# Kernel tuning notes

Hardware: AMD Instinct MI355X
Metric: run time of the kernel (lower is better)

## Reference

```python
import jax, jax.numpy as jnp
import numpy as np

NUM_HEADS = 16
HEAD_DIM = 64  # hidden_size 1024 / 16 heads


def setup_inputs() -> dict:
    key = jax.random.key(0)
    ks = jax.random.split(key, 9)
    B, T, H = 8, 4096, 1024
    s = 1.0 / np.sqrt(H)
    return {
        "hidden_states": jax.random.normal(ks[0], (B, T + 1, H), jnp.float32),
        "cell_state": jax.random.normal(ks[1], (B, H), jnp.float32),
        "Wq": jax.random.normal(ks[2], (H, H), jnp.float32) * s,
        "bq": jax.random.normal(ks[3], (H,), jnp.float32) * 0.02,
        "Wk": jax.random.normal(ks[4], (H, H), jnp.float32) * s,
        "bk": jax.random.normal(ks[5], (H,), jnp.float32) * 0.02,
        "Wv": jax.random.normal(ks[6], (H, H), jnp.float32) * s,
        "bv": jax.random.normal(ks[7], (H,), jnp.float32) * 0.02,
        "attention_mask": jax.random.randint(ks[8], (B, T), 0, 2, jnp.int32),
        "t": T,
    }


def reference(hidden_states, cell_state, Wq, bq, Wk, bk, Wv, bv, attention_mask, t):
    B, _, H = hidden_states.shape
    nh, hd = NUM_HEADS, HEAD_DIM
    # single-query projection: [B, H] -> [B, nh, hd]
    q = (cell_state @ Wq.T + bq).reshape(B, nh, hd)
    # key/value over first t positions: [B, t, H] -> [B, t, nh, hd]
    kv_in = hidden_states[:, :-1]
    k = (kv_in @ Wk.T + bk).reshape(B, t, nh, hd)
    v = (kv_in @ Wv.T + bv).reshape(B, t, nh, hd)
    # GEMV-like scores: [B, nh, t]
    scores = jnp.einsum("bhd,bthd->bht", q, k) / np.sqrt(hd)
    # mask out positions where attention_mask == 0 (intended semantics of
    # inf * eq(mask, 0) in the original, expressed without -inf*0 NaNs)
    mask_add = jnp.where(attention_mask == 0, -jnp.inf, 0.0)[:, None, :]
    probs = jax.nn.softmax(scores + mask_add, axis=-1)
    # dropout is identity in eval mode
    ctx = jnp.einsum("bht,bthd->bhd", probs, v)  # [B, nh, hd]
    return ctx.reshape(B, nh * hd)  # squeeze of [B, 1, H]
```

## Files before the change

kernel.cpp:

```cpp
#include <hip/hip_runtime.h>
#include <math.h>

#define BB 8
#define TT 4096
#define TP1 4097
#define HH 1024
#define NHD 16

__device__ __forceinline__ float dot4(const float4& a, const float4& b) {
  return a.x*b.x + a.y*b.y + a.z*b.z + a.w*b.w;
}

__global__ __launch_bounds__(256) void k_q(const float* __restrict__ cell,
                                           const float* __restrict__ Wq,
                                           const float* __restrict__ bq,
                                           float* __restrict__ qbuf) {
  __shared__ float cs[BB * HH];
  int tid = threadIdx.x;
  #pragma unroll
  for (int m = 0; m < 8; m++) {
    int idx4 = tid + (m << 8);
    ((float4*)cs)[idx4] = ((const float4*)cell)[idx4];
  }
  __syncthreads();
  int jj = tid >> 6, lane = tid & 63;
  int j = blockIdx.x * 4 + jj;
  float acc[BB];
  #pragma unroll
  for (int b = 0; b < BB; b++) acc[b] = 0.f;
  #pragma unroll
  for (int k = 0; k < 4; k++) {
    int i = (k << 8) + (lane << 2);
    float4 w = *(const float4*)&Wq[(size_t)j * HH + i];
    #pragma unroll
    for (int b = 0; b < BB; b++) acc[b] += dot4(w, *(const float4*)&cs[b * HH + i]);
  }
  #pragma unroll
  for (int b = 0; b < BB; b++) {
    acc[b] += __shfl_xor(acc[b], 1);  acc[b] += __shfl_xor(acc[b], 2);
    acc[b] += __shfl_xor(acc[b], 4);  acc[b] += __shfl_xor(acc[b], 8);
    acc[b] += __shfl_xor(acc[b], 16); acc[b] += __shfl_xor(acc[b], 32);
  }
  if (lane == 0) {
    float bqv = bq[j];
    #pragma unroll
    for (int b = 0; b < BB; b++) qbuf[b * HH + j] = 0.125f * (acc[b] + bqv);
  }
}

__global__ __launch_bounds__(256) void k_qwk(const float* __restrict__ qbuf,
                                             const float* __restrict__ Wk,
                                             const float* __restrict__ bk,
                                             float* __restrict__ qWkT,
                                             float* __restrict__ qbk) {
  __shared__ float q_s[BB * 64];
  __shared__ float red[4 * 64 * 9];
  int tid = threadIdx.x;
  int h = blockIdx.x >> 4, ic = blockIdx.x & 15;
  if (tid < 128) {
    int b = tid >> 4, dq = tid & 15;
    ((float4*)q_s)[tid] = ((const float4*)qbuf)[(b << 8) + (h << 4) + dq];
  }
  __syncthreads();
  int dg = tid >> 6, lane = tid & 63;
  int i = (ic << 6) + lane;
  float acc[BB];
  #pragma unroll
  for (int b = 0; b < BB; b++) acc[b] = 0.f;
  #pragma unroll
  for (int dd = 0; dd < 16; dd++) {
    int d = (dg << 4) + dd;
    float wk = Wk[(size_t)((h << 6) + d) * HH + i];
    #pragma unroll
    for (int b = 0; b < BB; b++) acc[b] += q_s[(b << 6) + d] * wk;
  }
  #pragma unroll
  for (int b = 0; b < BB; b++) red[((dg << 6) + lane) * 9 + b] = acc[b];
  __syncthreads();
  #pragma unroll
  for (int r = 0; r < 2; r++) {
    int o = tid + (r << 8);
    int il = o >> 3, b = o & 7;
    float s = 0.f;
    #pragma unroll
    for (int g = 0; g < 4; g++) s += red[((g << 6) + il) * 9 + b];
    qWkT[((size_t)(b << 10) + (ic << 6) + il) * NHD + h] = s;
  }
  if (ic == 0 && tid < 8) {
    float s = 0.f;
    for (int d = 0; d < 64; d++) s += q_s[(tid << 6) + d] * bk[(h << 6) + d];
    qbk[tid * NHD + h] = s;
  }
}

#define QT_OFF   0
#define KV_OFF   16384
#define E_OFF    32768
#define RED_OFF  33024
#define RED2_OFF 34048
#define QBK_OFF  34112
#define MSK_OFF  34128

__global__ __launch_bounds__(256, 1) void k_sctx(const float* __restrict__ hid,
                                                 const float* __restrict__ qWkT,
                                                 const float* __restrict__ qbk,
                                                 const int* __restrict__ mask,
                                                 float* __restrict__ ctxp,
                                                 float* __restrict__ Spart) {
  __shared__ float S[34192];
  int tid = threadIdx.x;
  int b = blockIdx.x >> 6, g = blockIdx.x & 63;
  int t0 = g << 6;
  int kq = tid >> 4, rg4 = tid & 15;
  int kqm = kq & 3;

  #pragma unroll
  for (int m = 0; m < 16; m++) {
    int idx = tid + (m << 8);
    float4 v = ((const float4*)qWkT)[((size_t)b << 12) + idx];
    *(float4*)&S[QT_OFF + (idx << 2)] = v;
  }
  if (tid < NHD) S[QBK_OFF + tid] = qbk[b * NHD + tid];
  if (tid < 64) S[MSK_OFF + tid] = (float)mask[b * TT + t0 + tid];

  const float* src = hid + ((size_t)b * TP1 + t0) * HH;
  float4 stg[16];
  #pragma unroll
  for (int m = 0; m < 16; m++)
    stg[m] = *(const float4*)&src[(size_t)m * HH + (tid << 2)];

  float4 acc4[16];
  #pragma unroll
  for (int h = 0; h < 16; h++) acc4[h] = make_float4(0.f, 0.f, 0.f, 0.f);
  float sp = 0.f;

  #pragma unroll 1
  for (int tt = 0; tt < 4; tt++) {
    #pragma unroll
    for (int m = 0; m < 16; m++)
      *(float4*)&S[KV_OFF + (((m << 8) + (tid ^ m)) << 2)] = stg[m];
    __syncthreads();

    float accs[16];
    #pragma unroll
    for (int k = 0; k < 16; k++) accs[k] = 0.f;
    #pragma unroll
    for (int qq = 0; qq < 16; qq++) {
      int q = (kq << 4) + qq;
      float4 kvq = *(const float4*)&S[KV_OFF + (((rg4 << 8) + (q ^ rg4)) << 2)];
      #pragma unroll
      for (int c = 0; c < 4; c++) {
        float kvv = (&kvq.x)[c];
        int i16 = ((q << 2) + c) << 4;
        #pragma unroll
        for (int j = 0; j < 4; j++) {
          int s = j ^ kqm;
          float4 qv = *(const float4*)&S[QT_OFF + i16 + (s << 2)];
          accs[(j << 2) + 0] += kvv * qv.x;
          accs[(j << 2) + 1] += kvv * qv.y;
          accs[(j << 2) + 2] += kvv * qv.z;
          accs[(j << 2) + 3] += kvv * qv.w;
        }
      }
    }
    {
      float tmp[16];
      #pragma unroll
      for (int j = 0; j < 4; j++)
        #pragma unroll
        for (int c = 0; c < 4; c++)
          tmp[(j << 2) + c] = __shfl_xor(accs[((j ^ 1) << 2) + c], 16);
      #pragma unroll
      for (int k = 0; k < 16; k++) accs[k] += tmp[k];
      #pragma unroll
      for (int j = 0; j < 4; j++)
        #pragma unroll
        for (int c = 0; c < 4; c++)
          tmp[(j << 2) + c] = __shfl_xor(accs[((j ^ 2) << 2) + c], 32);
      #pragma unroll
      for (int k = 0; k < 16; k++) accs[k] += tmp[k];
    }
    if ((tid & 48) == 0) {
      int w = tid >> 6;
      #pragma unroll
      for (int j = 0; j < 4; j++)
        *(float4*)&S[RED_OFF + (w << 8) + (rg4 << 4) + (j << 2)] =
            make_float4(accs[(j << 2)], accs[(j << 2) + 1],
                        accs[(j << 2) + 2], accs[(j << 2) + 3]);
    }
    __syncthreads();

    {
      int rge = tid >> 4, he = tid & 15;
      float sv = S[RED_OFF + (rge << 4) + he] + S[RED_OFF + 256 + (rge << 4) + he] +
                 S[RED_OFF + 512 + (rge << 4) + he] + S[RED_OFF + 768 + (rge << 4) + he];
      sv += S[QBK_OFF + he];
      float mkf = S[MSK_OFF + (tt << 4) + rge];
      float ev = (mkf != 0.f) ? __expf(sv) : 0.f;
      S[E_OFF + (rge << 4) + he] = ev;
      sp += ev;
    }
    __syncthreads();

    if (tt < 3) {
      const float* s2 = src + ((size_t)((tt + 1) << 4)) * HH;
      #pragma unroll
      for (int m = 0; m < 16; m++)
        stg[m] = *(const float4*)&s2[(size_t)m * HH + (tid << 2)];
    }

    #pragma unroll
    for (int r = 0; r < 16; r++) {
      float4 kvq = *(const float4*)&S[KV_OFF + (((r << 8) + (tid ^ r)) << 2)];
      float4 e0 = *(const float4*)&S[E_OFF + (r << 4)];
      float4 e1 = *(const float4*)&S[E_OFF + (r << 4) + 4];
      float4 e2 = *(const float4*)&S[E_OFF + (r << 4) + 8];
      float4 e3 = *(const float4*)&S[E_OFF + (r << 4) + 12];
      #define PVH(hh, ev) \
        acc4[hh].x += kvq.x * (ev); acc4[hh].y += kvq.y * (ev); \
        acc4[hh].z += kvq.z * (ev); acc4[hh].w += kvq.w * (ev);
      PVH(0, e0.x)  PVH(1, e0.y)  PVH(2, e0.z)  PVH(3, e0.w)
      PVH(4, e1.x)  PVH(5, e1.y)  PVH(6, e1.z)  PVH(7, e1.w)
      PVH(8, e2.x)  PVH(9, e2.y)  PVH(10, e2.z) PVH(11, e2.w)
      PVH(12, e3.x) PVH(13, e3.y) PVH(14, e3.z) PVH(15, e3.w)
      #undef PVH
    }
    __syncthreads();
  }

  {
    float* cp = ctxp + ((((size_t)b * 64 + g) * 16) << 10) + (tid << 2);
    #pragma unroll
    for (int h = 0; h < 16; h++)
      *(float4*)&cp[(size_t)h << 10] = acc4[h];
  }

  {
    sp += __shfl_xor(sp, 16);
    sp += __shfl_xor(sp, 32);
    int w = tid >> 6;
    if ((tid & 48) == 0) S[RED2_OFF + (w << 4) + (tid & 15)] = sp;
  }
  __syncthreads();
  if (tid < 16) {
    float s = S[RED2_OFF + tid] + S[RED2_OFF + 16 + tid] +
              S[RED2_OFF + 32 + tid] + S[RED2_OFF + 48 + tid];
    Spart[(((size_t)b << 6) + g) * NHD + tid] = s;
  }
}

__global__ void k_sinv(const float* __restrict__ Spart, float* __restrict__ Sinv) {
  int tid = threadIdx.x;
  int b = tid >> 4, h = tid & 15;
  float s = 0.f;
  #pragma unroll 8
  for (int c = 0; c < 64; c++) s += Spart[(size_t)((b << 6) + c) * NHD + h];
  Sinv[tid] = 1.f / s;
}

__global__ __launch_bounds__(256) void k_reduce(const float* __restrict__ ctxp,
                                                float* __restrict__ ctxin) {
  int tid = threadIdx.x;
  int b = blockIdx.x >> 4, h = blockIdx.x & 15;
  const float4* cp4 = (const float4*)ctxp;
  float4 s = make_float4(0.f, 0.f, 0.f, 0.f);
  #pragma unroll 8
  for (int g = 0; g < 64; g++) {
    float4 v = cp4[((((size_t)b * 64 + g) * 16 + h) << 8) + tid];
    s.x += v.x; s.y += v.y; s.z += v.z; s.w += v.w;
  }
  ((float4*)ctxin)[(((size_t)(b << 4) + h) << 8) + tid] = s;
}

__global__ __launch_bounds__(256) void k_out(const float* __restrict__ Wv,
                                             const float* __restrict__ bv,
                                             const float* __restrict__ ctxin,
                                             const float* __restrict__ Sinv,
                                             float* __restrict__ out) {
  __shared__ float cs[BB * HH];
  int tid = threadIdx.x;
  int h = blockIdx.x >> 4;
  int j0 = blockIdx.x * 4;
  #pragma unroll
  for (int m = 0; m < 8; m++) {
    int idx4 = tid + (m << 8);
    int b = idx4 >> 8, i4 = idx4 & 255;
    ((float4*)cs)[idx4] = ((const float4*)ctxin)[(((b << 4) + h) << 8) + i4];
  }
  __syncthreads();
  int jj = tid >> 6, lane = tid & 63;
  int j = j0 + jj;
  float acc[BB];
  #pragma unroll
  for (int b = 0; b < BB; b++) acc[b] = 0.f;
  #pragma unroll
  for (int k = 0; k < 4; k++) {
    int i = (k << 8) + (lane << 2);
    float4 w = *(const float4*)&Wv[(size_t)j * HH + i];
    #pragma unroll
    for (int b = 0; b < BB; b++) acc[b] += dot4(w, *(const float4*)&cs[b * HH + i]);
  }
  #pragma unroll
  for (int b = 0; b < BB; b++) {
    acc[b] += __shfl_xor(acc[b], 1);  acc[b] += __shfl_xor(acc[b], 2);
    acc[b] += __shfl_xor(acc[b], 4);  acc[b] += __shfl_xor(acc[b], 8);
    acc[b] += __shfl_xor(acc[b], 16); acc[b] += __shfl_xor(acc[b], 32);
  }
  if (lane == 0) {
    float bvj = bv[j];
    #pragma unroll
    for (int b = 0; b < BB; b++)
      out[b * HH + j] = Sinv[b * NHD + h] * acc[b] + bvj;
  }
}

extern "C" void kernel_launch(void* const* d_in, const int* in_sizes, int n_in,
                              void* d_out, int out_size, void* d_ws, size_t ws_size,
                              hipStream_t stream) {
  const float* hid  = (const float*)d_in[0];
  const float* cell = (const float*)d_in[1];
  const float* Wq   = (const float*)d_in[2];
  const float* bq   = (const float*)d_in[3];
  const float* Wk   = (const float*)d_in[4];
  const float* bk   = (const float*)d_in[5];
  const float* Wv   = (const float*)d_in[6];
  const float* bv   = (const float*)d_in[7];
  const int*  mask  = (const int*)d_in[8];
  float* out = (float*)d_out;

  float* ws = (float*)d_ws;
  float* qbuf    = ws;
  float* qWkT    = ws + 8192;
  float* qbk     = ws + 139264;
  float* Spart   = ws + 139392;
  float* Sinv    = ws + 147584;
  float* ctxin   = ws + 147712;
  float* ctxp    = ws + 278784;

  hipLaunchKernelGGL(k_q,      dim3(256), dim3(256), 0, stream, cell, Wq, bq, qbuf);
  hipLaunchKernelGGL(k_qwk,    dim3(256), dim3(256), 0, stream, qbuf, Wk, bk, qWkT, qbk);
  hipLaunchKernelGGL(k_sctx,   dim3(512), dim3(256), 0, stream, hid, qWkT, qbk, mask, ctxp, Spart);
  hipLaunchKernelGGL(k_sinv,   dim3(1),   dim3(128), 0, stream, Spart, Sinv);
  hipLaunchKernelGGL(k_reduce, dim3(128), dim3(256), 0, stream, ctxp, ctxin);
  hipLaunchKernelGGL(k_out,    dim3(256), dim3(256), 0, stream, Wv, bv, ctxin, Sinv, out);
}
```

Before: 307.5 us.

## Restructure score/context kernel into two passes with 512-thread blocks

Rewrites k_sctx so each block first computes scores over all 64 positions, streaming 256-column chunks of hidden states, with 8 waves each taking a slice of the reduction dimension. qWkT is now read directly from global memory instead of being staged in LDS. Scores are then reduced across waves, exponentiated and masked, and a second pass re-streams the hidden-state chunks to accumulate context using only 4 of the 8 waves. This frees LDS and raises occupancy, at the cost of reading hidden states twice (probably served from cache) and leaving half the waves idle in the context pass.

```diff
diff --git a/kernel.cpp b/kernel.cpp
--- a/kernel.cpp
+++ b/kernel.cpp
@@ -93,159 +93,151 @@
   }
 }
 
-#define QT_OFF   0
-#define KV_OFF   16384
-#define E_OFF    32768
-#define RED_OFF  33024
-#define RED2_OFF 34048
-#define QBK_OFF  34112
-#define MSK_OFF  34128
-
-__global__ __launch_bounds__(256, 1) void k_sctx(const float* __restrict__ hid,
+__global__ __launch_bounds__(512, 4) void k_sctx(const float* __restrict__ hid,
                                                  const float* __restrict__ qWkT,
                                                  const float* __restrict__ qbk,
                                                  const int* __restrict__ mask,
                                                  float* __restrict__ ctxp,
                                                  float* __restrict__ Spart) {
-  __shared__ float S[34192];
+  __shared__ float KV[16640];
+  __shared__ float E[1280];
   int tid = threadIdx.x;
   int b = blockIdx.x >> 6, g = blockIdx.x & 63;
   int t0 = g << 6;
-  int kq = tid >> 4, rg4 = tid & 15;
-  int kqm = kq & 3;
-
-  #pragma unroll
-  for (int m = 0; m < 16; m++) {
-    int idx = tid + (m << 8);
-    float4 v = ((const float4*)qWkT)[((size_t)b << 12) + idx];
-    *(float4*)&S[QT_OFF + (idx << 2)] = v;
-  }
-  if (tid < NHD) S[QBK_OFF + tid] = qbk[b * NHD + tid];
-  if (tid < 64) S[MSK_OFF + tid] = (float)mask[b * TT + t0 + tid];
-
+  int w = __builtin_amdgcn_readfirstlane(tid >> 6);
+  int lane = tid & 63;
   const float* src = hid + ((size_t)b * TP1 + t0) * HH;
-  float4 stg[16];
-  #pragma unroll
-  for (int m = 0; m < 16; m++)
-    stg[m] = *(const float4*)&src[(size_t)m * HH + (tid << 2)];
-
-  float4 acc4[16];
-  #pragma unroll
-  for (int h = 0; h < 16; h++) acc4[h] = make_float4(0.f, 0.f, 0.f, 0.f);
-  float sp = 0.f;
-
-  #pragma unroll 1
-  for (int tt = 0; tt < 4; tt++) {
-    #pragma unroll
-    for (int m = 0; m < 16; m++)
-      *(float4*)&S[KV_OFF + (((m << 8) + (tid ^ m)) << 2)] = stg[m];
+
+  int sr = tid >> 3, si8 = tid & 7;
+  const float* gs = src + (size_t)sr * HH + (si8 << 2);
+  float* kvw = KV + sr * 260 + (si8 << 2);
+
+  float4 stg[8];
+  #pragma unroll
+  for (int m = 0; m < 8; m++) stg[m] = *(const float4*)(gs + (m << 5));
+  #pragma unroll
+  for (int m = 0; m < 8; m++) *(float4*)(kvw + (m << 5)) = stg[m];
+  __syncthreads();
+
+  float acc[16];
+  #pragma unroll
+  for (int h = 0; h < 16; h++) acc[h] = 0.f;
+  const float* qb = qWkT + ((size_t)b << 14);
+  const float* kvr = KV + lane * 260 + (w << 5);
+
+  for (int c = 0; c < 4; c++) {
+    if (c < 3) {
+      const float* gs2 = gs + ((c + 1) << 8);
+      #pragma unroll
+      for (int m = 0; m < 8; m++) stg[m] = *(const float4*)(gs2 + (m << 5));
+    }
+    int i0 = (c << 8) + (w << 5);
+    #pragma unroll
+    for (int s = 0; s < 8; s++) {
+      float4 kvq = *(const float4*)(kvr + (s << 2));
+      const float* qp = qb + ((size_t)(i0 + (s << 2)) << 4);
+      #pragma unroll
+      for (int ii = 0; ii < 4; ii++) {
+        float kvv = (ii == 0) ? kvq.x : (ii == 1) ? kvq.y : (ii == 2) ? kvq.z : kvq.w;
+        const float* qi = qp + (ii << 4);
+        float4 q0 = *(const float4*)(qi);
+        float4 q1 = *(const float4*)(qi + 4);
+        float4 q2 = *(const float4*)(qi + 8);
+        float4 q3 = *(const float4*)(qi + 12);
+        acc[0]  += kvv * q0.x;  acc[1]  += kvv * q0.y;
+        acc[2]  += kvv * q0.z;  acc[3]  += kvv * q0.w;
+        acc[4]  += kvv * q1.x;  acc[5]  += kvv * q1.y;
+        acc[6]  += kvv * q1.z;  acc[7]  += kvv * q1.w;
+        acc[8]  += kvv * q2.x;  acc[9]  += kvv * q2.y;
+        acc[10] += kvv * q2.z;  acc[11] += kvv * q2.w;
+        acc[12] += kvv * q3.x;  acc[13] += kvv * q3.y;
+        acc[14] += kvv * q3.z;  acc[15] += kvv * q3.w;
+      }
+    }
     __syncthreads();
-
-    float accs[16];
-    #pragma unroll
-    for (int k = 0; k < 16; k++) accs[k] = 0.f;
-    #pragma unroll
-    for (int qq = 0; qq < 16; qq++) {
-      int q = (kq << 4) + qq;
-      float4 kvq = *(const float4*)&S[KV_OFF + (((rg4 << 8) + (q ^ rg4)) << 2)];
-      #pragma unroll
-      for (int c = 0; c < 4; c++) {
-        float kvv = (&kvq.x)[c];
-        int i16 = ((q << 2) + c) << 4;
-        #pragma unroll
-        for (int j = 0; j < 4; j++) {
-          int s = j ^ kqm;
-          float4 qv = *(const float4*)&S[QT_OFF + i16 + (s << 2)];
-          accs[(j << 2) + 0] += kvv * qv.x;
-          accs[(j << 2) + 1] += kvv * qv.y;
-          accs[(j << 2) + 2] += kvv * qv.z;
-          accs[(j << 2) + 3] += kvv * qv.w;
-        }
+    if (c < 3) {
+      #pragma unroll
+      for (int m = 0; m < 8; m++) *(float4*)(kvw + (m << 5)) = stg[m];
+    }
+    __syncthreads();
+  }
+
+  #pragma unroll
+  for (int m = 0; m < 8; m++) stg[m] = *(const float4*)(gs + (m << 5));
+
+  {
+    float* rp = KV + w * 1088 + lane * 17;
+    #pragma unroll
+    for (int h = 0; h < 16; h++) rp[h] = acc[h];
+  }
+  __syncthreads();
+
+  {
+    float s1 = 0.f, s2 = 0.f;
+    #pragma unroll
+    for (int ww = 0; ww < 8; ww++) {
+      s1 += KV[ww * 1088 + lane * 17 + w];
+      s2 += KV[ww * 1088 + lane * 17 + w + 8];
+    }
+    s1 += qbk[b * NHD + w];
+    s2 += qbk[b * NHD + w + 8];
+    int mk = mask[b * TT + t0 + lane];
+    float e1 = mk ? __expf(s1) : 0.f;
+    float e2 = mk ? __expf(s2) : 0.f;
+    E[lane * 20 + w] = e1;
+    E[lane * 20 + w + 8] = e2;
+    float sp1 = e1, sp2 = e2;
+    #pragma unroll
+    for (int m2 = 1; m2 < 64; m2 <<= 1) {
+      sp1 += __shfl_xor(sp1, m2);
+      sp2 += __shfl_xor(sp2, m2);
+    }
+    if (lane == 0) {
+      Spart[(((size_t)b << 6) + g) * NHD + w] = sp1;
+      Spart[(((size_t)b << 6) + g) * NHD + w + 8] = sp2;
+    }
+  }
+  __syncthreads();
+
+  #pragma unroll
+  for (int m = 0; m < 8; m++) *(float4*)(kvw + (m << 5)) = stg[m];
+  __syncthreads();
+
+  int hq = w & 3;
+  for (int c = 0; c < 4; c++) {
+    if (c < 3) {
+      const float* gs2 = gs + ((c + 1) << 8);
+      #pragma unroll
+      for (int m = 0; m < 8; m++) stg[m] = *(const float4*)(gs2 + (m << 5));
+    }
+    if (w < 4) {
+      float4 p0 = make_float4(0.f, 0.f, 0.f, 0.f);
+      float4 p1 = make_float4(0.f, 0.f, 0.f, 0.f);
+      float4 p2 = make_float4(0.f, 0.f, 0.f, 0.f);
+      float4 p3 = make_float4(0.f, 0.f, 0.f, 0.f);
+      const float* kvp = KV + (lane << 2);
+      const float* ep = E + (hq << 2);
+      #pragma unroll 8
+      for (int r = 0; r < 64; r++) {
+        float4 kvq = *(const float4*)(kvp + r * 260);
+        float4 ev  = *(const float4*)(ep + r * 20);
+        p0.x += kvq.x * ev.x; p0.y += kvq.y * ev.x; p0.z += kvq.z * ev.x; p0.w += kvq.w * ev.x;
+        p1.x += kvq.x * ev.y; p1.y += kvq.y * ev.y; p1.z += kvq.z * ev.y; p1.w += kvq.w * ev.y;
+        p2.x += kvq.x * ev.z; p2.y += kvq.y * ev.z; p2.z += kvq.z * ev.z; p2.w += kvq.w * ev.z;
+        p3.x += kvq.x * ev.w; p3.y += kvq.y * ev.w; p3.z += kvq.z * ev.w; p3.w += kvq.w * ev.w;
       }
-    }
-    {
-      float tmp[16];
-      #pragma unroll
-      for (int j = 0; j < 4; j++)
-        #pragma unroll
-        for (int c = 0; c < 4; c++)
-          tmp[(j << 2) + c] = __shfl_xor(accs[((j ^ 1) << 2) + c], 16);
-      #pragma unroll
-      for (int k = 0; k < 16; k++) accs[k] += tmp[k];
-      #pragma unroll
-      for (int j = 0; j < 4; j++)
-        #pragma unroll
-        for (int c = 0; c < 4; c++)
-          tmp[(j << 2) + c] = __shfl_xor(accs[((j ^ 2) << 2) + c], 32);
-      #pragma unroll
-      for (int k = 0; k < 16; k++) accs[k] += tmp[k];
-    }
-    if ((tid & 48) == 0) {
-      int w = tid >> 6;
-      #pragma unroll
-      for (int j = 0; j < 4; j++)
-        *(float4*)&S[RED_OFF + (w << 8) + (rg4 << 4) + (j << 2)] =
-            make_float4(accs[(j << 2)], accs[(j << 2) + 1],
-                        accs[(j << 2) + 2], accs[(j << 2) + 3]);
+      float* cp = ctxp + ((((size_t)(b << 6) + g) * NHD + (hq << 2)) << 10) + (c << 8) + (lane << 2);
+      *(float4*)(cp)        = p0;
+      *(float4*)(cp + 1024) = p1;
+      *(float4*)(cp + 2048) = p2;
+      *(float4*)(cp + 3072) = p3;
     }
     __syncthreads();
-
-    {
-      int rge = tid >> 4, he = tid & 15;
-      float sv = S[RED_OFF + (rge << 4) + he] + S[RED_OFF + 256 + (rge << 4) + he] +
-                 S[RED_OFF + 512 + (rge << 4) + he] + S[RED_OFF + 768 + (rge << 4) + he];
-      sv += S[QBK_OFF + he];
-      float mkf = S[MSK_OFF + (tt << 4) + rge];
-      float ev = (mkf != 0.f) ? __expf(sv) : 0.f;
-      S[E_OFF + (rge << 4) + he] = ev;
-      sp += ev;
+    if (c < 3) {
+      #pragma unroll
+      for (int m = 0; m < 8; m++) *(float4*)(kvw + (m << 5)) = stg[m];
     }
     __syncthreads();
-
-    if (tt < 3) {
-      const float* s2 = src + ((size_t)((tt + 1) << 4)) * HH;
-      #pragma unroll
-      for (int m = 0; m < 16; m++)
-        stg[m] = *(const float4*)&s2[(size_t)m * HH + (tid << 2)];
-    }
-
-    #pragma unroll
-    for (int r = 0; r < 16; r++) {
-      float4 kvq = *(const float4*)&S[KV_OFF + (((r << 8) + (tid ^ r)) << 2)];
-      float4 e0 = *(const float4*)&S[E_OFF + (r << 4)];
-      float4 e1 = *(const float4*)&S[E_OFF + (r << 4) + 4];
-      float4 e2 = *(const float4*)&S[E_OFF + (r << 4) + 8];
-      float4 e3 = *(const float4*)&S[E_OFF + (r << 4) + 12];
-      #define PVH(hh, ev) \
-        acc4[hh].x += kvq.x * (ev); acc4[hh].y += kvq.y * (ev); \
-        acc4[hh].z += kvq.z * (ev); acc4[hh].w += kvq.w * (ev);
-      PVH(0, e0.x)  PVH(1, e0.y)  PVH(2, e0.z)  PVH(3, e0.w)
-      PVH(4, e1.x)  PVH(5, e1.y)  PVH(6, e1.z)  PVH(7, e1.w)
-      PVH(8, e2.x)  PVH(9, e2.y)  PVH(10, e2.z) PVH(11, e2.w)
-      PVH(12, e3.x) PVH(13, e3.y) PVH(14, e3.z) PVH(15, e3.w)
-      #undef PVH
-    }
-    __syncthreads();
-  }
-
-  {
-    float* cp = ctxp + ((((size_t)b * 64 + g) * 16) << 10) + (tid << 2);
-    #pragma unroll
-    for (int h = 0; h < 16; h++)
-      *(float4*)&cp[(size_t)h << 10] = acc4[h];
-  }
-
-  {
-    sp += __shfl_xor(sp, 16);
-    sp += __shfl_xor(sp, 32);
-    int w = tid >> 6;
-    if ((tid & 48) == 0) S[RED2_OFF + (w << 4) + (tid & 15)] = sp;
-  }
-  __syncthreads();
-  if (tid < 16) {
-    float s = S[RED2_OFF + tid] + S[RED2_OFF + 16 + tid] +
-              S[RED2_OFF + 32 + tid] + S[RED2_OFF + 48 + tid];
-    Spart[(((size_t)b << 6) + g) * NHD + tid] = s;
   }
 }
 
@@ -339,7 +331,7 @@
 
   hipLaunchKernelGGL(k_q,      dim3(256), dim3(256), 0, stream, cell, Wq, bq, qbuf);
   hipLaunchKernelGGL(k_qwk,    dim3(256), dim3(256), 0, stream, qbuf, Wk, bk, qWkT, qbk);
-  hipLaunchKernelGGL(k_sctx,   dim3(512), dim3(256), 0, stream, hid, qWkT, qbk, mask, ctxp, Spart);
+  hipLaunchKernelGGL(k_sctx,   dim3(512), dim3(512), 0, stream, hid, qWkT, qbk, mask, ctxp, Spart);
   hipLaunchKernelGGL(k_sinv,   dim3(1),   dim3(128), 0, stream, Spart, Sinv);
   hipLaunchKernelGGL(k_reduce, dim3(128), dim3(256), 0, stream, ctxp, ctxin);
   hipLaunchKernelGGL(k_out,    dim3(256), dim3(256), 0, stream, Wv, bv, ctxin, Sinv, out);
```

New measurement: 342.6 us. 11.4% more time.
